# Kernel tuning notes

Measured on AMD Instinct MI355X. Metric: run time of the kernel, lower is better.

## Reference

```python
import jax, jax.numpy as jnp
import numpy as np

B, C, N = 2, 128, 512
EPS = 1e-5


def group_norm(x, gamma, beta, groups):
    # x: [B, Ch, H, W], normalize per group over (Ch//groups, H, W)
    b, ch, h, w = x.shape
    xg = x.reshape(b, groups, -1)
    m = xg.mean(axis=-1, keepdims=True)
    v = xg.var(axis=-1, keepdims=True)
    xg = (xg - m) * jax.lax.rsqrt(v + EPS)
    x = xg.reshape(b, ch, h, w)
    return x * gamma[None, :, None, None] + beta[None, :, None, None]


def setup_inputs() -> dict:
    key = jax.random.key(0)
    ks = jax.random.split(key, 12)
    s1 = 1.0 / np.sqrt(C)
    s2 = 1.0 / np.sqrt(2 * C)
    return {
        "feat": jax.random.normal(ks[0], (B, C, N), jnp.float32),
        "Wk": jax.random.normal(ks[1], (C, C), jnp.float32) * s1,
        "bk": jnp.zeros((C,), jnp.float32),
        "Wq": jax.random.normal(ks[2], (C, C), jnp.float32) * s1,
        "bq": jnp.zeros((C,), jnp.float32),
        "Wv": jax.random.normal(ks[3], (C, C), jnp.float32) * s1,
        "bv": jnp.zeros((C,), jnp.float32),
        "gn_v_g": jnp.ones((C,), jnp.float32),
        "gn_v_b": jnp.zeros((C,), jnp.float32),
        "gn1_g": jnp.ones((2 * C,), jnp.float32),
        "gn1_b": jnp.zeros((2 * C,), jnp.float32),
        "W1": jax.random.normal(ks[4], (C, 2 * C), jnp.float32) * s2,
        "b1": jnp.zeros((C,), jnp.float32),
        "gn2_g": jnp.ones((C,), jnp.float32),
        "gn2_b": jnp.zeros((C,), jnp.float32),
        "W2": jax.random.normal(ks[5], (C, C), jnp.float32) * s1,
        "b2": jnp.zeros((C,), jnp.float32),
    }


def reference(feat, Wk, bk, Wq, bq, Wv, bv, gn_v_g, gn_v_b,
              gn1_g, gn1_b, W1, b1, gn2_g, gn2_b, W2, b2):
    # feat: [B, C, N]
    n = feat.shape[-1]
    # 1x1 conv projections == channel matmuls
    k = jnp.einsum('oc,bcn->bon', Wk, feat) + bk[None, :, None]
    q = jnp.einsum('oc,bcn->bon', Wq, feat) + bq[None, :, None]
    v = jnp.einsum('oc,bcn->bon', Wv, feat) + bv[None, :, None]
    # value path: conv -> GroupNorm(min(32,C)) -> ReLU
    v = group_norm(v[:, :, :, None], gn_v_g, gn_v_b, min(32, C))[:, :, :, 0]
    v = jax.nn.relu(v)
    # pairwise broadcast-concat: [B, 2C, N, N] (query varies over dim -2, key over dim -1)
    qx = jnp.broadcast_to(q[:, :, :, None], (q.shape[0], C, n, n))
    kx = jnp.broadcast_to(k[:, :, None, :], (k.shape[0], C, n, n))
    pair = jnp.concatenate([qx, kx], axis=1)
    # weight_conv: ReLU -> GN(2C) -> conv(2C->C) -> ReLU -> GN(C) -> conv(C->C)
    h = jax.nn.relu(pair)
    h = group_norm(h, gn1_g, gn1_b, min(32, 2 * C))
    h = jnp.einsum('oc,bcij->boij', W1, h) + b1[None, :, None, None]
    h = jax.nn.relu(h)
    h = group_norm(h, gn2_g, gn2_b, min(32, C))
    score = jnp.einsum('oc,bcij->boij', W2, h) + b2[None, :, None, None]
    weight = jax.nn.softmax(score, axis=-1)  # [B, C, N, N]
    # faithful to torch code: value broadcast over last dim, sum over last dim
    out = (v[:, :, :, None] * weight).sum(axis=-1)  # [B, C, N]
    return out
```

## Files before the change

kernel.cpp:

```cpp
#include <hip/hip_runtime.h>


#define BATCH  2
#define CH     128
#define NPOS   512
#define GROUPS 32
#define CPG    4
#define GEPS   1e-5f

__global__ __launch_bounds__(256) void vpath_kernel(
    const float* __restrict__ feat,
    const float* __restrict__ Wv,
    const float* __restrict__ bv,
    const float* __restrict__ gam,
    const float* __restrict__ bet,
    float* __restrict__ out)
{
    const int b   = blockIdx.x >> 5;
    const int g   = blockIdx.x & 31;
    const int ch0 = g * CPG;
    const int t   = threadIdx.x;

    __shared__ float w[CPG][CH];
    __shared__ float red[8];
    __shared__ float stats[2];

    {
        const int i0 = t * 2;
        #pragma unroll
        for (int k = 0; k < 2; ++k) {
            int i = i0 + k;
            int j = i >> 7;
            int c = i & 127;
            w[j][c] = Wv[(ch0 + j) * CH + c];
        }
    }
    __syncthreads();

    float acc0[CPG] = {0.f, 0.f, 0.f, 0.f};
    float acc1[CPG] = {0.f, 0.f, 0.f, 0.f};
    const float2* fp =
        reinterpret_cast<const float2*>(feat + (size_t)b * CH * NPOS) + t;
    #pragma unroll 4
    for (int c = 0; c < CH; ++c) {
        float2 f = fp[c * (NPOS / 2)];
        #pragma unroll
        for (int j = 0; j < CPG; ++j) {
            float wv = w[j][c];
            acc0[j] = fmaf(wv, f.x, acc0[j]);
            acc1[j] = fmaf(wv, f.y, acc1[j]);
        }
    }

    float s = 0.f, s2 = 0.f;
    #pragma unroll
    for (int j = 0; j < CPG; ++j) {
        float bias = bv[ch0 + j];
        acc0[j] += bias;
        acc1[j] += bias;
        s  += acc0[j] + acc1[j];
        s2 += acc0[j] * acc0[j] + acc1[j] * acc1[j];
    }

    #pragma unroll
    for (int off = 32; off > 0; off >>= 1) {
        s  += __shfl_down(s, off);
        s2 += __shfl_down(s2, off);
    }
    const int wave = t >> 6;
    if ((t & 63) == 0) {
        red[wave]     = s;
        red[wave + 4] = s2;
    }
    __syncthreads();
    if (t == 0) {
        float S  = red[0] + red[1] + red[2] + red[3];
        float S2 = red[4] + red[5] + red[6] + red[7];
        const float inv_n = 1.0f / (float)(CPG * NPOS);
        float m   = S * inv_n;
        float var = S2 * inv_n - m * m;
        stats[0] = m;
        stats[1] = rsqrtf(var + GEPS);
    }
    __syncthreads();
    const float m = stats[0];
    const float r = stats[1];

    float2* op =
        reinterpret_cast<float2*>(out + (size_t)(b * CH + ch0) * NPOS) + t;
    #pragma unroll
    for (int j = 0; j < CPG; ++j) {
        float ga = gam[ch0 + j];
        float be = bet[ch0 + j];
        float2 y;
        y.x = fmaxf((acc0[j] - m) * r * ga + be, 0.0f);
        y.y = fmaxf((acc1[j] - m) * r * ga + be, 0.0f);
        op[j * (NPOS / 2)] = y;
    }
}

extern "C" void kernel_launch(void* const* d_in, const int* in_sizes, int n_in,
                              void* d_out, int out_size, void* d_ws, size_t ws_size,
                              hipStream_t stream) {
    const float* feat = (const float*)d_in[0];
    const float* Wv   = (const float*)d_in[5];
    const float* bv   = (const float*)d_in[6];
    const float* gng  = (const float*)d_in[7];
    const float* gnb  = (const float*)d_in[8];
    float* out = (float*)d_out;

    vpath_kernel<<<dim3(BATCH * GROUPS), dim3(256), 0, stream>>>(
        feat, Wv, bv, gng, gnb, out);
}
```

Before: 94.03 us.

## Split value projection and group norm into two kernels with chunked grid

The fused projection plus GroupNorm kernel, which ran one block per (batch, group), is split in two. The first kernel uses four position chunks per group and one wave per channel, writes the projected values and per-chunk partial sums to workspace. The second kernel combines the partials into mean and rstd, then applies the affine transform and ReLU. This raises the grid from 64 to 256 blocks to fill more compute units, at the cost of a second launch and a round trip of the intermediate through global memory.

```diff
diff --git a/kernel.cpp b/kernel.cpp
--- a/kernel.cpp
+++ b/kernel.cpp
@@ -1,102 +1,116 @@
 #include <hip/hip_runtime.h>
 
 
-#define BATCH  2
-#define CH     128
-#define NPOS   512
-#define GROUPS 32
-#define CPG    4
-#define GEPS   1e-5f
+#define BATCH   2
+#define CH      128
+#define NPOS    512
+#define GROUPS  32
+#define CPG     4
+#define CHUNKS  4
+#define CHUNK_N (NPOS / CHUNKS)
+#define GEPS    1e-5f
 
-__global__ __launch_bounds__(256) void vpath_kernel(
+__global__ __launch_bounds__(256) void vproj_kernel(
     const float* __restrict__ feat,
     const float* __restrict__ Wv,
     const float* __restrict__ bv,
-    const float* __restrict__ gam,
-    const float* __restrict__ bet,
-    float* __restrict__ out)
+    float* __restrict__ vbuf,
+    float* __restrict__ partial)
 {
-    const int b   = blockIdx.x >> 5;
-    const int g   = blockIdx.x & 31;
-    const int ch0 = g * CPG;
-    const int t   = threadIdx.x;
+    const int blk   = blockIdx.x;
+    const int chunk = blk & (CHUNKS - 1);
+    const int g     = (blk >> 2) & (GROUPS - 1);
+    const int b     = blk >> 7;
+    const int ch0   = g * CPG;
+    const int t     = threadIdx.x;
+    const int wave  = t >> 6;
+    const int lane  = t & 63;
 
     __shared__ float w[CPG][CH];
     __shared__ float red[8];
-    __shared__ float stats[2];
 
     {
-        const int i0 = t * 2;
-        #pragma unroll
-        for (int k = 0; k < 2; ++k) {
-            int i = i0 + k;
-            int j = i >> 7;
-            int c = i & 127;
-            w[j][c] = Wv[(ch0 + j) * CH + c];
-        }
+        int i = t * 2;
+        int j = i >> 7, c = i & (CH - 1);
+        w[j][c] = Wv[(ch0 + j) * CH + c];
+        ++i; j = i >> 7; c = i & (CH - 1);
+        w[j][c] = Wv[(ch0 + j) * CH + c];
     }
     __syncthreads();
 
-    float acc0[CPG] = {0.f, 0.f, 0.f, 0.f};
-    float acc1[CPG] = {0.f, 0.f, 0.f, 0.f};
-    const float2* fp =
-        reinterpret_cast<const float2*>(feat + (size_t)b * CH * NPOS) + t;
-    #pragma unroll 4
+    const int j = wave;
+    float acc0 = 0.f, acc1 = 0.f;
+    const float2* fp = reinterpret_cast<const float2*>(
+        feat + (size_t)b * CH * NPOS + chunk * CHUNK_N) + lane;
+    #pragma unroll 16
     for (int c = 0; c < CH; ++c) {
-        float2 f = fp[c * (NPOS / 2)];
-        #pragma unroll
-        for (int j = 0; j < CPG; ++j) {
-            float wv = w[j][c];
-            acc0[j] = fmaf(wv, f.x, acc0[j]);
-            acc1[j] = fmaf(wv, f.y, acc1[j]);
-        }
+        float2 f  = fp[c * (NPOS / 2)];
+        float  wv = w[j][c];
+        acc0 = fmaf(wv, f.x, acc0);
+        acc1 = fmaf(wv, f.y, acc1);
     }
+    const float bias = bv[ch0 + j];
+    acc0 += bias;
+    acc1 += bias;
 
-    float s = 0.f, s2 = 0.f;
-    #pragma unroll
-    for (int j = 0; j < CPG; ++j) {
-        float bias = bv[ch0 + j];
-        acc0[j] += bias;
-        acc1[j] += bias;
-        s  += acc0[j] + acc1[j];
-        s2 += acc0[j] * acc0[j] + acc1[j] * acc1[j];
-    }
+    float2* vp = reinterpret_cast<float2*>(
+        vbuf + ((size_t)(b * CH + ch0 + j)) * NPOS + chunk * CHUNK_N) + lane;
+    *vp = make_float2(acc0, acc1);
 
+    float s  = acc0 + acc1;
+    float s2 = acc0 * acc0 + acc1 * acc1;
     #pragma unroll
     for (int off = 32; off > 0; off >>= 1) {
         s  += __shfl_down(s, off);
         s2 += __shfl_down(s2, off);
     }
-    const int wave = t >> 6;
-    if ((t & 63) == 0) {
-        red[wave]     = s;
-        red[wave + 4] = s2;
-    }
+    if (lane == 0) { red[wave] = s; red[wave + 4] = s2; }
     __syncthreads();
     if (t == 0) {
         float S  = red[0] + red[1] + red[2] + red[3];
         float S2 = red[4] + red[5] + red[6] + red[7];
-        const float inv_n = 1.0f / (float)(CPG * NPOS);
-        float m   = S * inv_n;
-        float var = S2 * inv_n - m * m;
-        stats[0] = m;
-        stats[1] = rsqrtf(var + GEPS);
+        float* p = partial + (size_t)((b * GROUPS + g) * CHUNKS + chunk) * 2;
+        p[0] = S;
+        p[1] = S2;
     }
-    __syncthreads();
-    const float m = stats[0];
-    const float r = stats[1];
+}
 
-    float2* op =
-        reinterpret_cast<float2*>(out + (size_t)(b * CH + ch0) * NPOS) + t;
-    #pragma unroll
-    for (int j = 0; j < CPG; ++j) {
-        float ga = gam[ch0 + j];
-        float be = bet[ch0 + j];
-        float2 y;
-        y.x = fmaxf((acc0[j] - m) * r * ga + be, 0.0f);
-        y.y = fmaxf((acc1[j] - m) * r * ga + be, 0.0f);
-        op[j * (NPOS / 2)] = y;
-    }
+__global__ __launch_bounds__(256) void gnorm_kernel(
+    const float* __restrict__ vbuf,
+    const float* __restrict__ partial,
+    const float* __restrict__ gam,
+    const float* __restrict__ bet,
+    float* __restrict__ out)
+{
+    const int blk   = blockIdx.x;
+    const int chunk = blk & (CHUNKS - 1);
+    const int g     = (blk >> 2) & (GROUPS - 1);
+    const int b     = blk >> 7;
+    const int ch0   = g * CPG;
+    const int t     = threadIdx.x;
+    const int j     = t >> 6;
+    const int lane  = t & 63;
+
+    const float* p = partial + (size_t)((b * GROUPS + g) * CHUNKS) * 2;
+    float S  = p[0] + p[2] + p[4] + p[6];
+    float S2 = p[1] + p[3] + p[5] + p[7];
+    const float inv_n = 1.0f / (float)(CPG * NPOS);
+    float m = S * inv_n;
+    float r = rsqrtf(S2 * inv_n - m * m + GEPS);
+
+    const float2* vp = reinterpret_cast<const float2*>(
+        vbuf + ((size_t)(b * CH + ch0 + j)) * NPOS + chunk * CHUNK_N) + lane;
+    float2 v = *vp;
+
+    float ga = gam[ch0 + j] * r;
+    float be = fmaf(-m, ga, bet[ch0 + j]);
+    float2 y;
+    y.x = fmaxf(fmaf(v.x, ga, be), 0.0f);
+    y.y = fmaxf(fmaf(v.y, ga, be), 0.0f);
+
+    float2* op = reinterpret_cast<float2*>(
+        out + ((size_t)(b * CH + ch0 + j)) * NPOS + chunk * CHUNK_N) + lane;
+    *op = y;
 }
 
 extern "C" void kernel_launch(void* const* d_in, const int* in_sizes, int n_in,
@@ -109,6 +123,12 @@
     const float* gnb  = (const float*)d_in[8];
     float* out = (float*)d_out;
 
-    vpath_kernel<<<dim3(BATCH * GROUPS), dim3(256), 0, stream>>>(
-        feat, Wv, bv, gng, gnb, out);
+    float* vbuf    = (float*)d_ws;
+    float* partial = vbuf + (size_t)BATCH * CH * NPOS;
+
+    const dim3 grid(BATCH * GROUPS * CHUNKS);
+    const dim3 blockDim3(256);
+
+    vproj_kernel<<<grid, blockDim3, 0, stream>>>(feat, Wv, bv, vbuf, partial);
+    gnorm_kernel<<<grid, blockDim3, 0, stream>>>(vbuf, partial, gng, gnb, out);
 }
```

Measured after the change: 90.31 us. 1.04x faster.
